# Optimization experiments

Hardware: AMD Instinct MI355X
Metric: run time of the kernel (lower is better)

The kernel has to match this reference:

```python
import jax, jax.numpy as jnp
import numpy as np

K = 20          # neighbors
EPS = 1e-5      # BatchNorm eps
SLOPE = 0.2     # LeakyReLU negative slope


def setup_inputs() -> dict:
    key = jax.random.key(0)
    k1, k2 = jax.random.split(key)
    B, C, N, O = 8, 64, 4096, 64
    x = jax.random.normal(k1, (B, C, N), dtype=jnp.float32)
    # 1x1 Conv2d(2C -> O, bias=False) kernel, squeezed to (O, 2C)
    W = jax.random.normal(k2, (O, 2 * C), dtype=jnp.float32) * 0.05
    gamma = jnp.ones((O,), jnp.float32)   # BN weight
    beta = jnp.zeros((O,), jnp.float32)   # BN bias
    return {"x": x, "W": W, "gamma": gamma, "beta": beta}


def _edgeconv(x, W, gamma, beta):
    B, C, N = x.shape
    xt = jnp.transpose(x, (0, 2, 1))                       # (B, N, C)
    # KNN on negative squared distance (matches torch topk of -dist)
    xx = jnp.sum(x * x, axis=1)                            # (B, N)
    inner = jnp.einsum('bnc,bmc->bnm', xt, xt)             # (B, N, N)
    neg_dist = 2.0 * inner - xx[:, :, None] - xx[:, None, :]
    _, idx = jax.lax.top_k(neg_dist, K)                    # (B, N, K) int32
    # gather neighbor features: nbr[b,n,k,c] = xt[b, idx[b,n,k], c]
    nbr = xt[jnp.arange(B)[:, None, None], idx]            # (B, N, K, C)
    center = jnp.broadcast_to(xt[:, :, None, :], (B, N, K, C))
    edge = jnp.concatenate([nbr - center, center], axis=-1)  # (B, N, K, 2C)
    # 1x1 conv == channel matmul
    y = jnp.einsum('bnkc,oc->bnko', edge, W)               # (B, N, K, O)
    # BatchNorm2d (training mode: batch statistics over B,N,K per channel)
    mean = jnp.mean(y, axis=(0, 1, 2))
    var = jnp.var(y, axis=(0, 1, 2))
    yn = (y - mean) * jax.lax.rsqrt(var + EPS) * gamma + beta
    ya = jnp.where(yn >= 0, yn, SLOPE * yn)                # LeakyReLU(0.2)
    out = jnp.max(ya, axis=2)                              # max over k -> (B, N, O)
    return jnp.transpose(out, (0, 2, 1))                   # (B, O, N)


def reference(x, W, gamma, beta):
    return _edgeconv(x, W, gamma, beta)
```

## Files before the change

kernel.cpp:

```cpp
#include <hip/hip_runtime.h>
#include <hip/hip_bf16.h>
#include <math.h>

#define B 8
#define C 64
#define NN 4096
#define O 64
#define KNN 20

typedef float f32x4 __attribute__((ext_vector_type(4)));
typedef short short8_t __attribute__((ext_vector_type(8)));

__device__ inline uint32_t fkey(float f) {
    uint32_t u = __float_as_uint(f);
    return u ^ (((uint32_t)((int32_t)u >> 31)) | 0x80000000u);
}

__device__ inline uint32_t med3u(uint32_t a, uint32_t b, uint32_t c) {
    uint32_t r;
    asm("v_med3_u32 %0, %1, %2, %3" : "=v"(r) : "v"(a), "v"(b), "v"(c));
    return r;
}
__device__ inline uint32_t umax(uint32_t a, uint32_t b) { return a > b ? a : b; }
__device__ inline uint32_t umin(uint32_t a, uint32_t b) { return a < b ? a : b; }

__device__ inline uint32_t minall16(uint32_t v) {
    uint32_t t;
    t = (uint32_t)__builtin_amdgcn_update_dpp(0, (int)v, 0x140, 0xF, 0xF, true);
    v = umin(v, t);
    t = (uint32_t)__builtin_amdgcn_update_dpp(0, (int)v, 0x141, 0xF, 0xF, true);
    v = umin(v, t);
    t = (uint32_t)__builtin_amdgcn_update_dpp(0, (int)v, 0x4E, 0xF, 0xF, true);
    v = umin(v, t);
    t = (uint32_t)__builtin_amdgcn_update_dpp(0, (int)v, 0xB1, 0xF, 0xF, true);
    v = umin(v, t);
    return v;
}


__global__ __launch_bounds__(256) void k1_split(const float* __restrict__ x,
                                                float* __restrict__ xt,
                                                __hip_bfloat16* __restrict__ xh,
                                                float* __restrict__ xx) {
    __shared__ float tile[64][65];
    int b  = blockIdx.x / (NN / 64);
    int n0 = (blockIdx.x % (NN / 64)) * 64;
    int t = threadIdx.x;
    #pragma unroll
    for (int it = 0; it < 16; ++it) {
        int i = it * 256 + t;
        int c = i >> 6, n = i & 63;
        tile[c][n] = x[(size_t)b * C * NN + (size_t)c * NN + n0 + n];
    }
    __syncthreads();
    #pragma unroll
    for (int it = 0; it < 16; ++it) {
        int i = it * 256 + t;
        int n = i >> 6, c = i & 63;
        float v = tile[c][n];
        xt[((size_t)(b * NN + n0 + n)) * C + c] = v;
        int tl   = (n0 + n) >> 4;
        int r    = n & 15;
        int half = c >> 5, cc = c & 31;
        int grp  = cc >> 3, e = cc & 7;
        size_t ta = (size_t)b * NN * 64 + (size_t)tl * 1024 + half * 512
                  + grp * 128 + r * 8 + e;
        xh[ta] = __float2bfloat16(v);
    }
    if (t < 64) {
        float s = 0.f;
        #pragma unroll
        for (int c = 0; c < 64; ++c) { float v = tile[c][t]; s = fmaf(v, v, s); }
        xx[(size_t)b * NN + t + n0] = s;
    }
}

__global__ __launch_bounds__(256) void k2_knn(const __hip_bfloat16* __restrict__ xh,
                                              const float* __restrict__ xt,
                                              const float* __restrict__ xx,
                                              int* __restrict__ idx) {
    int b     = blockIdx.x & 7;
    int qbase = (blockIdx.x >> 3) << 6;
    int t = threadIdx.x;
    int w = t >> 6, lane = t & 63;
    int laneid = lane & 15, grp = lane >> 4;
    int n0w = qbase + w * 16;

    const __hip_bfloat16* xhtb = xh + (size_t)b * NN * 64;
    const float* xxb = xx + (size_t)b * NN;
    const float* xtb = xt + (size_t)b * NN * 64;

    const __hip_bfloat16* lp = xhtb + lane * 8;

    short8_t Ah0 = *(const short8_t*)(lp + (size_t)(n0w >> 4) * 1024);
    short8_t Ah1 = *(const short8_t*)(lp + (size_t)(n0w >> 4) * 1024 + 512);

    float bq[4];
    #pragma unroll
    for (int j = 0; j < 4; ++j) bq[j] = -2.f - xxb[n0w + grp * 4 + j];

    uint32_t qq[4][12];
    #pragma unroll
    for (int j = 0; j < 4; ++j)
        #pragma unroll
        for (int i = 0; i < 12; ++i) qq[j][i] = 0xFFFFFFFFu;

    short8_t P00, P01, P10, P11, P20, P21, P30, P31;
    float Px0, Px1, Px2, Px3;
    P00 = *(const short8_t*)(lp);        P01 = *(const short8_t*)(lp + 512);
    P10 = *(const short8_t*)(lp + 1024); P11 = *(const short8_t*)(lp + 1536);
    P20 = *(const short8_t*)(lp + 2048); P21 = *(const short8_t*)(lp + 2560);
    P30 = *(const short8_t*)(lp + 3072); P31 = *(const short8_t*)(lp + 3584);
    Px0 = xxb[laneid];      Px1 = xxb[laneid + 16];
    Px2 = xxb[laneid + 32]; Px3 = xxb[laneid + 48];

#define SWEEP_BODY(PB0, PB1, PXX, K, PF, OFF)                                  \
    {                                                                          \
        float xxc = PXX;                                                       \
        f32x4 acc = {0.f, 0.f, 0.f, 0.f};                                      \
        acc = __builtin_amdgcn_mfma_f32_16x16x32_bf16(Ah0, PB0, acc, 0, 0, 0); \
        acc = __builtin_amdgcn_mfma_f32_16x16x32_bf16(Ah1, PB1, acc, 0, 0, 0); \
        PB0 = *(const short8_t*)(PF + OFF);                                    \
        PB1 = *(const short8_t*)(PF + OFF + 512);                              \
        PXX = xxb[ci0 + (4 + K) * 16];                                         \
        uint32_t ci = (uint32_t)(ci0 + K * 16);                                \
        _Pragma("unroll")                                                      \
        for (int j = 0; j < 4; ++j) {                                          \
            uint32_t u = __float_as_uint(fmaf(acc[j], 2.f, bq[j] - xxc));      \
            uint32_t nv = (u & 0xFFFFF000u) | ci;                              \
            _Pragma("unroll")                                                  \
            for (int i = 11; i >= 1; --i)                                      \
                qq[j][i] = med3u(qq[j][i - 1], qq[j][i], nv);                  \
            qq[j][0] = umin(qq[j][0], nv);                                     \
        }                                                                      \
    }

    #pragma unroll 1
    for (int tt = 0; tt < 256; tt += 4) {
        int ci0 = tt * 16 + laneid;
        const __hip_bfloat16* pf0 = lp + (size_t)(tt + 4) * 1024;
        const __hip_bfloat16* pf2 = pf0 + 2048;
        SWEEP_BODY(P00, P01, Px0, 0, pf0, 0)
        SWEEP_BODY(P10, P11, Px1, 1, pf0, 1024)
        SWEEP_BODY(P20, P21, Px2, 2, pf2, 0)
        SWEEP_BODY(P30, P31, Px3, 3, pf2, 1024)
    }
#undef SWEEP_BODY

    __shared__ uint32_t cand[4][16][33];
    __shared__ uint32_t rkk[4][16][33];
    __shared__ float qrow[4][16][68];

    #pragma unroll
    for (int i = 0; i < 16; ++i)
        qrow[w][i][lane] = xtb[(size_t)(n0w + i) * 64 + lane];

    #pragma unroll 1
    for (int r = 0; r < 32; ++r) {
        #pragma unroll
        for (int j = 0; j < 4; ++j) {
            uint32_t bk = minall16(qq[j][0]);
            bool win = (qq[j][0] == bk);
            #pragma unroll
            for (int i = 0; i < 11; ++i) qq[j][i] = win ? qq[j][i + 1] : qq[j][i];
            qq[j][11] = win ? 0xFFFFFFFFu : qq[j][11];
            if (laneid == 0) cand[w][grp * 4 + j][r] = bk & 4095u;
        }
    }
    __syncthreads();

    int rq = lane >> 2, rs = lane & 3;
    float qxx = xxb[n0w + rq];
    const float4* qr = (const float4*)qrow[w][rq];
    uint32_t ky[8], cl[8];
    #pragma unroll
    for (int e = 0; e < 8; ++e) {
        uint32_t col = cand[w][rq][rs + 4 * e];
        const float4* cr = (const float4*)(xtb + (size_t)col * 64);
        float a = 0.f;
        #pragma unroll
        for (int i = 0; i < 16; ++i) {
            float4 qv = qr[i], cv = cr[i];
            a = fmaf(qv.x, cv.x, a); a = fmaf(qv.y, cv.y, a);
            a = fmaf(qv.z, cv.z, a); a = fmaf(qv.w, cv.w, a);
        }
        float d = 2.f * a - qxx - xxb[col];
        ky[e] = fkey(d);
        cl[e] = col;
        rkk[w][rq][rs + 4 * e] = ky[e];
    }
    __syncthreads();

    int rank[8];
    #pragma unroll
    for (int e = 0; e < 8; ++e) rank[e] = 0;
    #pragma unroll
    for (int jj = 0; jj < 32; ++jj) {
        uint32_t kj = rkk[w][rq][jj], cj = cand[w][rq][jj];
        #pragma unroll
        for (int e = 0; e < 8; ++e)
            rank[e] += (kj > ky[e] || (kj == ky[e] && cj < cl[e])) ? 1 : 0;
    }
    size_t ob = ((size_t)(b * NN) + n0w + rq) * KNN;
    #pragma unroll
    for (int e = 0; e < 8; ++e)
        if (rank[e] < KNN) idx[ob + rank[e]] = (int)cl[e];
}

__global__ __launch_bounds__(256) void k3a_gemm(const float* __restrict__ xt,
                                                const float* __restrict__ W,
                                                float* __restrict__ Z,
                                                float* __restrict__ Z2) {
    __shared__ float W0t[64][65];
    __shared__ float W21t[64][65];
    __shared__ float xs[16][64];
    int t = threadIdx.x;
    #pragma unroll
    for (int it = 0; it < 16; ++it) {
        int i = it * 256 + t;
        int o = i >> 6, c = i & 63;
        float w0 = W[o * 128 + c];
        float w1 = W[o * 128 + 64 + c];
        W0t[c][o]  = w0;
        W21t[c][o] = w1 - w0;
    }
    int b  = blockIdx.x / (NN / 16);
    int nb = (blockIdx.x % (NN / 16)) * 16;
    #pragma unroll
    for (int it = 0; it < 4; ++it) {
        int i = it * 256 + t;
        int r = i >> 6, c = i & 63;
        xs[r][c] = xt[((size_t)(b * NN + nb + r)) * C + c];
    }
    __syncthreads();
    int o = t & 63, rg = t >> 6;
    #pragma unroll
    for (int rr = 0; rr < 4; ++rr) {
        int r = rg * 4 + rr;
        float z = 0.f, z2 = 0.f;
        #pragma unroll
        for (int c = 0; c < 64; ++c) {
            float xv = xs[r][c];
            z  = fmaf(xv, W0t[c][o],  z);
            z2 = fmaf(xv, W21t[c][o], z2);
        }
        size_t off = ((size_t)(b * NN + nb + r)) * 64 + o;
        Z[off]  = z;
        Z2[off] = z2;
    }
}

__global__ __launch_bounds__(256) void k3b_gather(const float* __restrict__ Z,
                                                  const float* __restrict__ Z2,
                                                  const int* __restrict__ idx,
                                                  float* __restrict__ maxY,
                                                  float* __restrict__ minY,
                                                  float* __restrict__ partials) {
    int t = threadIdx.x;
    int p = t >> 6, o = t & 63;
    int b = blockIdx.x & 7;
    int n = (blockIdx.x >> 3) * 4 + p;
    size_t base = (size_t)(b * NN + n);
    float z2 = Z2[base * 64 + o];
    __shared__ int sidx[4][KNN];
    if (o < KNN) sidx[p][o] = idx[base * KNN + o];
    __syncthreads();
    const float* Zb = Z + (size_t)b * NN * 64;
    float s1 = 0.f, s2 = 0.f, mx = -INFINITY, mn = INFINITY;
    #pragma unroll
    for (int k = 0; k < KNN; ++k) {
        float y = Zb[(size_t)sidx[p][k] * 64 + o] + z2;
        s1 += y;
        s2 = fmaf(y, y, s2);
        mx = fmaxf(mx, y);
        mn = fminf(mn, y);
    }
    maxY[base * 64 + o] = mx;
    minY[base * 64 + o] = mn;
    __shared__ float red[2][4][64];
    red[0][p][o] = s1;
    red[1][p][o] = s2;
    __syncthreads();
    if (t < 64) {
        float a = red[0][0][t] + red[0][1][t] + red[0][2][t] + red[0][3][t];
        float c = red[1][0][t] + red[1][1][t] + red[1][2][t] + red[1][3][t];
        partials[(size_t)blockIdx.x * 128 + t]      = a;
        partials[(size_t)blockIdx.x * 128 + 64 + t] = c;
    }
}

__global__ __launch_bounds__(256) void k4a_reduce(const float* __restrict__ partials,
                                                  float* __restrict__ partials2) {
    int g = blockIdx.x;
    int t = threadIdx.x;
    int col = t & 127, half = t >> 7;
    float s = 0.f;
    for (int r = half; r < 128; r += 2)
        s += partials[((size_t)g * 128 + r) * 128 + col];
    __shared__ float red[2][128];
    red[half][col] = s;
    __syncthreads();
    if (t < 128) partials2[(size_t)g * 128 + t] = red[0][t] + red[1][t];
}

__global__ __launch_bounds__(256) void k5_out(const float* __restrict__ partials2,
                                              const float* __restrict__ gamma,
                                              const float* __restrict__ beta,
                                              const float* __restrict__ maxY,
                                              const float* __restrict__ minY,
                                              float* __restrict__ out) {
    __shared__ float tile[64][65];
    __shared__ double red[128];
    __shared__ float sc[64], sh[64];
    int t = threadIdx.x;
    if (t < 128) {
        double s = 0.0;
        for (int i = 0; i < 64; ++i)
            s += (double)partials2[(size_t)i * 128 + t];
        red[t] = s;
    }
    __syncthreads();
    if (t < 64) {
        double a = red[t], c = red[64 + t];
        double M = (double)B * NN * KNN;
        double mean = a / M;
        double var  = c / M - mean * mean;
        float s = gamma[t] * rsqrtf((float)var + 1e-5f);
        sc[t] = s;
        sh[t] = beta[t] - (float)mean * s;
    }
    int b  = blockIdx.x / (NN / 64);
    int n0 = (blockIdx.x % (NN / 64)) * 64;
    __syncthreads();
    #pragma unroll
    for (int it = 0; it < 16; ++it) {
        int i = it * 256 + t;
        int nl = i >> 6, o = i & 63;
        size_t off = ((size_t)(b * NN + n0 + nl)) * 64 + o;
        float s = sc[o];
        float v = (s >= 0.f) ? maxY[off] : minY[off];
        v = fmaf(v, s, sh[o]);
        v = (v >= 0.f) ? v : 0.2f * v;
        tile[nl][o] = v;
    }
    __syncthreads();
    #pragma unroll
    for (int it = 0; it < 16; ++it) {
        int i = it * 256 + t;
        int o = i >> 6, nl = i & 63;
        out[((size_t)(b * O + o)) * NN + n0 + nl] = tile[nl][o];
    }
}

extern "C" void kernel_launch(void* const* d_in, const int* in_sizes, int n_in,
                              void* d_out, int out_size, void* d_ws, size_t ws_size,
                              hipStream_t stream) {
    const float* x     = (const float*)d_in[0];
    const float* W     = (const float*)d_in[1];
    const float* gamma = (const float*)d_in[2];
    const float* beta  = (const float*)d_in[3];
    float* out = (float*)d_out;

    float* ws = (float*)d_ws;
    float* xx = ws;
    float* xt = xx + (size_t)B * NN;
    __hip_bfloat16* xh = (__hip_bfloat16*)(xt + (size_t)B * NN * C);
    int*   idx = (int*)(xh + (size_t)B * NN * C);
    float* Z   = (float*)(idx + (size_t)B * NN * KNN);
    float* Z2  = Z + (size_t)B * NN * O;
    float* maxY = Z2 + (size_t)B * NN * O;
    float* minY = maxY + (size_t)B * NN * O;
    float* partials  = minY + (size_t)B * NN * O;
    float* partials2 = partials + (size_t)(B * NN / 4) * 128;

    k1_split<<<B * (NN / 64), 256, 0, stream>>>(x, xt, xh, xx);
    k2_knn<<<B * (NN / 64), 256, 0, stream>>>(xh, xt, xx, idx);
    k3a_gemm<<<B * (NN / 16), 256, 0, stream>>>(xt, W, Z, Z2);
    k3b_gather<<<B * (NN / 4), 256, 0, stream>>>(Z, Z2, idx, maxY, minY, partials);
    k4a_reduce<<<64, 256, 0, stream>>>(partials, partials2);
    k5_out<<<B * (NN / 64), 256, 0, stream>>>(partials2, gamma, beta, maxY, minY, out);
}
```

Before: 234.3 us.

## Stage candidate tiles through double-buffered shared memory in KNN sweep

```diff
diff --git a/kernel.cpp b/kernel.cpp
--- a/kernel.cpp
+++ b/kernel.cpp
@@ -105,51 +105,64 @@
         #pragma unroll
         for (int i = 0; i < 12; ++i) qq[j][i] = 0xFFFFFFFFu;
 
-    short8_t P00, P01, P10, P11, P20, P21, P30, P31;
-    float Px0, Px1, Px2, Px3;
-    P00 = *(const short8_t*)(lp);        P01 = *(const short8_t*)(lp + 512);
-    P10 = *(const short8_t*)(lp + 1024); P11 = *(const short8_t*)(lp + 1536);
-    P20 = *(const short8_t*)(lp + 2048); P21 = *(const short8_t*)(lp + 2560);
-    P30 = *(const short8_t*)(lp + 3072); P31 = *(const short8_t*)(lp + 3584);
-    Px0 = xxb[laneid];      Px1 = xxb[laneid + 16];
-    Px2 = xxb[laneid + 32]; Px3 = xxb[laneid + 48];
-
-#define SWEEP_BODY(PB0, PB1, PXX, K, PF, OFF)                                  \
-    {                                                                          \
-        float xxc = PXX;                                                       \
-        f32x4 acc = {0.f, 0.f, 0.f, 0.f};                                      \
-        acc = __builtin_amdgcn_mfma_f32_16x16x32_bf16(Ah0, PB0, acc, 0, 0, 0); \
-        acc = __builtin_amdgcn_mfma_f32_16x16x32_bf16(Ah1, PB1, acc, 0, 0, 0); \
-        PB0 = *(const short8_t*)(PF + OFF);                                    \
-        PB1 = *(const short8_t*)(PF + OFF + 512);                              \
-        PXX = xxb[ci0 + (4 + K) * 16];                                         \
-        uint32_t ci = (uint32_t)(ci0 + K * 16);                                \
-        _Pragma("unroll")                                                      \
-        for (int j = 0; j < 4; ++j) {                                          \
-            uint32_t u = __float_as_uint(fmaf(acc[j], 2.f, bq[j] - xxc));      \
-            uint32_t nv = (u & 0xFFFFF000u) | ci;                              \
-            _Pragma("unroll")                                                  \
-            for (int i = 11; i >= 1; --i)                                      \
-                qq[j][i] = med3u(qq[j][i - 1], qq[j][i], nv);                  \
-            qq[j][0] = umin(qq[j][0], nv);                                     \
-        }                                                                      \
-    }
-
-    #pragma unroll 1
-    for (int tt = 0; tt < 256; tt += 4) {
-        int ci0 = tt * 16 + laneid;
-        const __hip_bfloat16* pf0 = lp + (size_t)(tt + 4) * 1024;
-        const __hip_bfloat16* pf2 = pf0 + 2048;
-        SWEEP_BODY(P00, P01, Px0, 0, pf0, 0)
-        SWEEP_BODY(P10, P11, Px1, 1, pf0, 1024)
-        SWEEP_BODY(P20, P21, Px2, 2, pf2, 0)
-        SWEEP_BODY(P30, P31, Px3, 3, pf2, 1024)
-    }
-#undef SWEEP_BODY
-
+    __shared__ __align__(16) char stagebuf[2][8448];
     __shared__ uint32_t cand[4][16][33];
     __shared__ uint32_t rkk[4][16][33];
     __shared__ float qrow[4][16][68];
+
+    const char* gtiles = (const char*)xhtb;
+
+    {
+        const char* gs = gtiles + (size_t)w * 2048 + lane * 16;
+        float4 p0 = *(const float4*)gs;
+        float4 p1 = *(const float4*)(gs + 1024);
+        float pxx = xxb[lane];
+        char* sd = &stagebuf[0][0];
+        *(float4*)(sd + w * 2048 + lane * 16) = p0;
+        *(float4*)(sd + w * 2048 + 1024 + lane * 16) = p1;
+        *(float*)(sd + 8192 + lane * 4) = pxx;
+    }
+    __syncthreads();
+
+    #pragma unroll 1
+    for (int g = 0; g < 64; ++g) {
+        int cur = g & 1;
+        float4 r0, r1; float rxx;
+        bool pf = (g + 1 < 64);
+        if (pf) {
+            const char* gs = gtiles + (size_t)(g + 1) * 8192 + w * 2048 + lane * 16;
+            r0 = *(const float4*)gs;
+            r1 = *(const float4*)(gs + 1024);
+            rxx = xxb[(g + 1) * 64 + lane];
+        }
+        const char* sb = &stagebuf[cur][0];
+        #pragma unroll
+        for (int k = 0; k < 4; ++k) {
+            short8_t B0 = *(const short8_t*)(sb + k * 2048 + lane * 16);
+            short8_t B1 = *(const short8_t*)(sb + k * 2048 + 1024 + lane * 16);
+            float xxc = *(const float*)(sb + 8192 + (k * 16 + laneid) * 4);
+            f32x4 acc = {0.f, 0.f, 0.f, 0.f};
+            acc = __builtin_amdgcn_mfma_f32_16x16x32_bf16(Ah0, B0, acc, 0, 0, 0);
+            acc = __builtin_amdgcn_mfma_f32_16x16x32_bf16(Ah1, B1, acc, 0, 0, 0);
+            uint32_t ci = (uint32_t)(g * 64 + k * 16 + laneid);
+            #pragma unroll
+            for (int j = 0; j < 4; ++j) {
+                uint32_t u = __float_as_uint(fmaf(acc[j], 2.f, bq[j] - xxc));
+                uint32_t nv = (u & 0xFFFFF000u) | ci;
+                #pragma unroll
+                for (int i = 11; i >= 1; --i)
+                    qq[j][i] = med3u(qq[j][i - 1], qq[j][i], nv);
+                qq[j][0] = umin(qq[j][0], nv);
+            }
+        }
+        if (pf) {
+            char* sd = &stagebuf[cur ^ 1][0];
+            *(float4*)(sd + w * 2048 + lane * 16) = r0;
+            *(float4*)(sd + w * 2048 + 1024 + lane * 16) = r1;
+            *(float*)(sd + 8192 + lane * 4) = rxx;
+        }
+        __syncthreads();
+    }
 
     #pragma unroll
     for (int i = 0; i < 16; ++i)
```

Result: slower. 259.9 us (+10.9%).

## Process two query tiles per wave in KNN sweep to reuse candidate loads

Applied to the files above, without the earlier changes.

```diff
diff --git a/kernel.cpp b/kernel.cpp
--- a/kernel.cpp
+++ b/kernel.cpp
@@ -80,11 +80,11 @@
                                               const float* __restrict__ xx,
                                               int* __restrict__ idx) {
     int b     = blockIdx.x & 7;
-    int qbase = (blockIdx.x >> 3) << 6;
+    int qbase = (blockIdx.x >> 3) << 7;
     int t = threadIdx.x;
     int w = t >> 6, lane = t & 63;
     int laneid = lane & 15, grp = lane >> 4;
-    int n0w = qbase + w * 16;
+    int n0w = qbase + w * 32;
 
     const __hip_bfloat16* xhtb = xh + (size_t)b * NN * 64;
     const float* xxb = xx + (size_t)b * NN;
@@ -92,90 +92,100 @@
 
     const __hip_bfloat16* lp = xhtb + lane * 8;
 
-    short8_t Ah0 = *(const short8_t*)(lp + (size_t)(n0w >> 4) * 1024);
-    short8_t Ah1 = *(const short8_t*)(lp + (size_t)(n0w >> 4) * 1024 + 512);
-
-    float bq[4];
-    #pragma unroll
-    for (int j = 0; j < 4; ++j) bq[j] = -2.f - xxb[n0w + grp * 4 + j];
-
-    uint32_t qq[4][12];
+    short8_t Aa0 = *(const short8_t*)(lp + (size_t)(n0w >> 4) * 1024);
+    short8_t Aa1 = *(const short8_t*)(lp + (size_t)(n0w >> 4) * 1024 + 512);
+    short8_t Ab0 = *(const short8_t*)(lp + (size_t)((n0w + 16) >> 4) * 1024);
+    short8_t Ab1 = *(const short8_t*)(lp + (size_t)((n0w + 16) >> 4) * 1024 + 512);
+
+    float bqa[4], bqb[4];
+    #pragma unroll
+    for (int j = 0; j < 4; ++j) {
+        bqa[j] = -2.f - xxb[n0w + grp * 4 + j];
+        bqb[j] = -2.f - xxb[n0w + 16 + grp * 4 + j];
+    }
+
+    uint32_t qa[4][12], qb[4][12];
     #pragma unroll
     for (int j = 0; j < 4; ++j)
         #pragma unroll
-        for (int i = 0; i < 12; ++i) qq[j][i] = 0xFFFFFFFFu;
-
-    short8_t P00, P01, P10, P11, P20, P21, P30, P31;
-    float Px0, Px1, Px2, Px3;
+        for (int i = 0; i < 12; ++i) { qa[j][i] = 0xFFFFFFFFu; qb[j][i] = 0xFFFFFFFFu; }
+
+    short8_t P00, P01, P10, P11;
+    float Px0, Px1;
     P00 = *(const short8_t*)(lp);        P01 = *(const short8_t*)(lp + 512);
     P10 = *(const short8_t*)(lp + 1024); P11 = *(const short8_t*)(lp + 1536);
-    P20 = *(const short8_t*)(lp + 2048); P21 = *(const short8_t*)(lp + 2560);
-    P30 = *(const short8_t*)(lp + 3072); P31 = *(const short8_t*)(lp + 3584);
     Px0 = xxb[laneid];      Px1 = xxb[laneid + 16];
-    Px2 = xxb[laneid + 32]; Px3 = xxb[laneid + 48];
-
-#define SWEEP_BODY(PB0, PB1, PXX, K, PF, OFF)                                  \
-    {                                                                          \
-        float xxc = PXX;                                                       \
-        f32x4 acc = {0.f, 0.f, 0.f, 0.f};                                      \
-        acc = __builtin_amdgcn_mfma_f32_16x16x32_bf16(Ah0, PB0, acc, 0, 0, 0); \
-        acc = __builtin_amdgcn_mfma_f32_16x16x32_bf16(Ah1, PB1, acc, 0, 0, 0); \
-        PB0 = *(const short8_t*)(PF + OFF);                                    \
-        PB1 = *(const short8_t*)(PF + OFF + 512);                              \
-        PXX = xxb[ci0 + (4 + K) * 16];                                         \
-        uint32_t ci = (uint32_t)(ci0 + K * 16);                                \
-        _Pragma("unroll")                                                      \
-        for (int j = 0; j < 4; ++j) {                                          \
-            uint32_t u = __float_as_uint(fmaf(acc[j], 2.f, bq[j] - xxc));      \
-            uint32_t nv = (u & 0xFFFFF000u) | ci;                              \
-            _Pragma("unroll")                                                  \
-            for (int i = 11; i >= 1; --i)                                      \
-                qq[j][i] = med3u(qq[j][i - 1], qq[j][i], nv);                  \
-            qq[j][0] = umin(qq[j][0], nv);                                     \
-        }                                                                      \
+
+#define SWEEP_BODY(PB0, PB1, PXX, K, PF, OFF)                                   \
+    {                                                                           \
+        float xxc = PXX;                                                        \
+        f32x4 acca = {0.f, 0.f, 0.f, 0.f};                                      \
+        f32x4 accb = {0.f, 0.f, 0.f, 0.f};                                      \
+        acca = __builtin_amdgcn_mfma_f32_16x16x32_bf16(Aa0, PB0, acca, 0, 0, 0);\
+        accb = __builtin_amdgcn_mfma_f32_16x16x32_bf16(Ab0, PB0, accb, 0, 0, 0);\
+        acca = __builtin_amdgcn_mfma_f32_16x16x32_bf16(Aa1, PB1, acca, 0, 0, 0);\
+        accb = __builtin_amdgcn_mfma_f32_16x16x32_bf16(Ab1, PB1, accb, 0, 0, 0);\
+        PB0 = *(const short8_t*)(PF + OFF);                                     \
+        PB1 = *(const short8_t*)(PF + OFF + 512);                               \
+        PXX = xxb[ci0 + (2 + K) * 16];                                          \
+        uint32_t ci = (uint32_t)(ci0 + K * 16);                                 \
+        _Pragma("unroll")                                                       \
+        for (int j = 0; j < 4; ++j) {                                           \
+            uint32_t ua = __float_as_uint(fmaf(acca[j], 2.f, bqa[j] - xxc));    \
+            uint32_t nva = (ua & 0xFFFFF000u) | ci;                             \
+            _Pragma("unroll")                                                   \
+            for (int i = 11; i >= 1; --i)                                       \
+                qa[j][i] = med3u(qa[j][i - 1], qa[j][i], nva);                  \
+            qa[j][0] = umin(qa[j][0], nva);                                     \
+            uint32_t ub = __float_as_uint(fmaf(accb[j], 2.f, bqb[j] - xxc));    \
+            uint32_t nvb = (ub & 0xFFFFF000u) | ci;                             \
+            _Pragma("unroll")                                                   \
+            for (int i = 11; i >= 1; --i)                                       \
+                qb[j][i] = med3u(qb[j][i - 1], qb[j][i], nvb);                  \
+            qb[j][0] = umin(qb[j][0], nvb);                                     \
+        }                                                                       \
     }
 
     #pragma unroll 1
-    for (int tt = 0; tt < 256; tt += 4) {
+    for (int tt = 0; tt < 256; tt += 2) {
         int ci0 = tt * 16 + laneid;
-        const __hip_bfloat16* pf0 = lp + (size_t)(tt + 4) * 1024;
-        const __hip_bfloat16* pf2 = pf0 + 2048;
-        SWEEP_BODY(P00, P01, Px0, 0, pf0, 0)
-        SWEEP_BODY(P10, P11, Px1, 1, pf0, 1024)
-        SWEEP_BODY(P20, P21, Px2, 2, pf2, 0)
-        SWEEP_BODY(P30, P31, Px3, 3, pf2, 1024)
+        const __hip_bfloat16* pf = lp + (size_t)(tt + 2) * 1024;
+        SWEEP_BODY(P00, P01, Px0, 0, pf, 0)
+        SWEEP_BODY(P10, P11, Px1, 1, pf, 1024)
     }
 #undef SWEEP_BODY
 
-    __shared__ uint32_t cand[4][16][33];
-    __shared__ uint32_t rkk[4][16][33];
-    __shared__ float qrow[4][16][68];
-
-    #pragma unroll
-    for (int i = 0; i < 16; ++i)
-        qrow[w][i][lane] = xtb[(size_t)(n0w + i) * 64 + lane];
+    __shared__ uint32_t cand[4][32][33];
+    __shared__ uint32_t rkk[4][32][33];
 
     #pragma unroll 1
     for (int r = 0; r < 32; ++r) {
         #pragma unroll
         for (int j = 0; j < 4; ++j) {
-            uint32_t bk = minall16(qq[j][0]);
-            bool win = (qq[j][0] == bk);
+            uint32_t bk = minall16(qa[j][0]);
+            bool win = (qa[j][0] == bk);
             #pragma unroll
-            for (int i = 0; i < 11; ++i) qq[j][i] = win ? qq[j][i + 1] : qq[j][i];
-            qq[j][11] = win ? 0xFFFFFFFFu : qq[j][11];
+            for (int i = 0; i < 11; ++i) qa[j][i] = win ? qa[j][i + 1] : qa[j][i];
+            qa[j][11] = win ? 0xFFFFFFFFu : qa[j][11];
             if (laneid == 0) cand[w][grp * 4 + j][r] = bk & 4095u;
+
+            uint32_t bk2 = minall16(qb[j][0]);
+            bool win2 = (qb[j][0] == bk2);
+            #pragma unroll
+            for (int i = 0; i < 11; ++i) qb[j][i] = win2 ? qb[j][i + 1] : qb[j][i];
+            qb[j][11] = win2 ? 0xFFFFFFFFu : qb[j][11];
+            if (laneid == 0) cand[w][16 + grp * 4 + j][r] = bk2 & 4095u;
         }
     }
     __syncthreads();
 
-    int rq = lane >> 2, rs = lane & 3;
+    int rq = lane >> 1, rs = lane & 1;
     float qxx = xxb[n0w + rq];
-    const float4* qr = (const float4*)qrow[w][rq];
-    uint32_t ky[8], cl[8];
-    #pragma unroll
-    for (int e = 0; e < 8; ++e) {
-        uint32_t col = cand[w][rq][rs + 4 * e];
+    const float4* qr = (const float4*)(xtb + (size_t)(n0w + rq) * 64);
+    uint32_t ky[16], cl[16];
+    #pragma unroll
+    for (int e = 0; e < 16; ++e) {
+        uint32_t col = cand[w][rq][rs + 2 * e];
         const float4* cr = (const float4*)(xtb + (size_t)col * 64);
         float a = 0.f;
         #pragma unroll
@@ -187,23 +197,23 @@
         float d = 2.f * a - qxx - xxb[col];
         ky[e] = fkey(d);
         cl[e] = col;
-        rkk[w][rq][rs + 4 * e] = ky[e];
-    }
-    __syncthreads();
-
-    int rank[8];
-    #pragma unroll
-    for (int e = 0; e < 8; ++e) rank[e] = 0;
+        rkk[w][rq][rs + 2 * e] = ky[e];
+    }
+    __syncthreads();
+
+    int rank[16];
+    #pragma unroll
+    for (int e = 0; e < 16; ++e) rank[e] = 0;
     #pragma unroll
     for (int jj = 0; jj < 32; ++jj) {
         uint32_t kj = rkk[w][rq][jj], cj = cand[w][rq][jj];
         #pragma unroll
-        for (int e = 0; e < 8; ++e)
+        for (int e = 0; e < 16; ++e)
             rank[e] += (kj > ky[e] || (kj == ky[e] && cj < cl[e])) ? 1 : 0;
     }
     size_t ob = ((size_t)(b * NN) + n0w + rq) * KNN;
     #pragma unroll
-    for (int e = 0; e < 8; ++e)
+    for (int e = 0; e < 16; ++e)
         if (rank[e] < KNN) idx[ob + rank[e]] = (int)cl[e];
 }
 
@@ -374,7 +384,7 @@
     float* partials2 = partials + (size_t)(B * NN / 4) * 128;
 
     k1_split<<<B * (NN / 64), 256, 0, stream>>>(x, xt, xh, xx);
-    k2_knn<<<B * (NN / 64), 256, 0, stream>>>(xh, xt, xx, idx);
+    k2_knn<<<B * (NN / 128), 256, 0, stream>>>(xh, xt, xx, idx);
     k3a_gemm<<<B * (NN / 16), 256, 0, stream>>>(xt, W, Z, Z2);
     k3b_gather<<<B * (NN / 4), 256, 0, stream>>>(Z, Z2, idx, maxY, minY, partials);
     k4a_reduce<<<64, 256, 0, stream>>>(partials, partials2);
```

After: 272.9 us. +16.5%, slower.
